# Performance work log

Hardware: AMD Instinct MI355X
Metric: run time of the kernel (lower is better)

The kernel has to match this reference:

```python
import jax, jax.numpy as jnp
import numpy as np

N_ATOMS = 4096
HSIZE = 128
N_HEADS = 8
D_K = HSIZE // N_HEADS


def setup_inputs() -> dict:
    key = jax.random.key(0)
    ks = jax.random.split(key, 11)
    s = 1.0 / np.sqrt(HSIZE)
    return {
        "query": jax.random.normal(ks[0], (N_ATOMS, HSIZE), dtype=jnp.float32),
        "key": jax.random.normal(ks[1], (N_ATOMS, HSIZE), dtype=jnp.float32),
        "value": jax.random.normal(ks[2], (N_ATOMS, HSIZE), dtype=jnp.float32),
        "mask": jax.random.randint(ks[3], (N_ATOMS, N_ATOMS), 0, 2, dtype=jnp.int32),
        "Wq": jax.random.normal(ks[4], (HSIZE, HSIZE), dtype=jnp.float32) * s,
        "bq": jnp.zeros((HSIZE,), dtype=jnp.float32),
        "Wk": jax.random.normal(ks[5], (HSIZE, HSIZE), dtype=jnp.float32) * s,
        "bk": jnp.zeros((HSIZE,), dtype=jnp.float32),
        "Wv": jax.random.normal(ks[6], (HSIZE, HSIZE), dtype=jnp.float32) * s,
        "bv": jnp.zeros((HSIZE,), dtype=jnp.float32),
        "Wo": jax.random.normal(ks[7], (HSIZE, HSIZE), dtype=jnp.float32) * s,
    }


def _mha(query, key, value, mask, Wq, bq, Wk, bk, Wv, bv, Wo):
    n = query.shape[0]
    # project and split heads: [n, hsize] -> [H, n, d_k]
    def heads(x, W, b):
        return (x @ W.T + b).reshape(n, N_HEADS, D_K).transpose(1, 0, 2)
    q = heads(query, Wq, bq)
    k = heads(key, Wk, bk)
    v = heads(value, Wv, bv)
    scale = 1.0 / jnp.sqrt(jnp.asarray(D_K, q.dtype))
    scores = jnp.einsum("hnd,hmd->hnm", q, k) * scale  # [H, n, n]
    scores = jnp.where(mask[None, :, :] == 0, jnp.asarray(-1e9, scores.dtype), scores)
    p_attn = jax.nn.softmax(scores, axis=-1)
    x = jnp.einsum("hnm,hmd->hnd", p_attn, v)  # [H, n, d_k]
    x = x.transpose(1, 0, 2).reshape(n, HSIZE)  # merge heads
    return x @ Wo.T  # output_linear has bias=False


def reference(query, key, value, mask, Wq, bq, Wk, bk, Wv, bv, Wo):
    return _mha(query, key, value, mask, Wq, bq, Wk, bk, Wv, bv, Wo)
```

## Files before the change

### kernel.cpp

```cpp
#include <hip/hip_runtime.h>

#define NA 4096
#define HS 128
#define PSTR 72
#define CSTR 136

typedef unsigned short u16;
typedef unsigned long long u64;
using bf16x8  = __attribute__((ext_vector_type(8))) short;
using f32x4   = __attribute__((ext_vector_type(4))) float;
using ushort8 = __attribute__((ext_vector_type(8))) unsigned short;

#define QSCALE 0.18033688011112042f

static __device__ __forceinline__ u16 f2bf(float f) {
    unsigned u = __builtin_bit_cast(unsigned, f);
    u += 0x7FFFu + ((u >> 16) & 1u);
    return (u16)(u >> 16);
}

__global__ __launch_bounds__(256) void cvt_w(
    const float* __restrict__ Wq, const float* __restrict__ Wk,
    const float* __restrict__ Wv, const float* __restrict__ Wo,
    const float* __restrict__ bq, const float* __restrict__ bk,
    const float* __restrict__ bv, const int* __restrict__ mask,
    u16* __restrict__ Wf, float* __restrict__ bb, u64* __restrict__ Mp)
{
    const int bx = blockIdx.x;
    const int t = threadIdx.x;
    if (bx < 64) {
        const int gid = bx * 256 + t;
        const int e = gid * 4;
        const int mat = e >> 14, off = e & 16383;
        const float* src = (mat == 0) ? Wq : (mat == 1) ? Wk : (mat == 2) ? Wv : Wo;
        const float s = (mat == 0) ? QSCALE : 1.0f;
        float4 v = *(const float4*)(src + off);
        ushort4 o;
        o.x = f2bf(v.x * s); o.y = f2bf(v.y * s);
        o.z = f2bf(v.z * s); o.w = f2bf(v.w * s);
        const int j = off >> 7, k0 = off & 127;
        const int j0 = j >> 4, c = j & 15, kk = k0 >> 5, q = (k0 >> 3) & 3;
        const int tgt = mat * 16384 + ((j0 * 4 + kk) * 16 + c) * 32 + q * 8 + (k0 & 7);
        *(ushort4*)(Wf + tgt) = o;
        if (gid < 128)      bb[gid] = bq[gid] * QSCALE;
        else if (gid < 256) bb[gid] = bk[gid - 128];
        else if (gid < 384) bb[gid] = bv[gid - 256];
    } else {
        const int mb = bx - 64;
        const int wv = t >> 6, lane = t & 63;
        const int row = mb * 4 + wv;
        const int* mrow = mask + (size_t)row * NA;
        u64* orow = Mp + (size_t)row * 64;
#pragma unroll 8
        for (int w = 0; w < 64; ++w) {
            u64 b = __ballot(mrow[w * 64 + lane] != 0);
            if (lane == 0) orow[w] = b;
        }
    }
}

__global__ __launch_bounds__(256) void proj_mfma(
    const float* __restrict__ Xq, const float* __restrict__ Xk, const float* __restrict__ Xv,
    const u16* __restrict__ Wf, const float* __restrict__ bb,
    u16* __restrict__ Qbh, u16* __restrict__ Kbh, u16* __restrict__ VtB)
{
    const int mat = blockIdx.y;
    const float* X = (mat == 0) ? Xq : (mat == 1) ? Xk : Xv;
    const u16* Wm = Wf + mat * 16384;
    const float* bm = bb + mat * 128;
    const int r0b = blockIdx.x * 32;

    __shared__ __align__(16) u16 Xs[32 * CSTR];
    __shared__ __align__(16) u16 Cs[32 * CSTR];

    const int t = threadIdx.x;

    {
        const int r = t >> 3, cb = (t & 7) * 16;
        const float* Xr = X + (size_t)(r0b + r) * HS + cb;
#pragma unroll
        for (int seg = 0; seg < 4; ++seg) {
            float4 f = *(const float4*)(Xr + seg * 4);
            ushort4 u;
            u.x = f2bf(f.x); u.y = f2bf(f.y); u.z = f2bf(f.z); u.w = f2bf(f.w);
            *(ushort4*)(Xs + r * CSTR + cb + seg * 4) = u;
        }
    }
    __syncthreads();

    const int wv = t >> 6, lane = t & 63;
    const int c = lane & 15, q = lane >> 4;
    const int rw = (wv & 1) * 16;
    const int j0b = (wv >> 1) * 4;

    bf16x8 af[4];
#pragma unroll
    for (int kk = 0; kk < 4; ++kk)
        af[kk] = *(const bf16x8*)(Xs + (rw + c) * CSTR + kk * 32 + q * 8);

    const f32x4 zero = {0.f, 0.f, 0.f, 0.f};
#pragma unroll
    for (int jj = 0; jj < 4; ++jj) {
        const int j0 = j0b + jj;
        f32x4 acc = zero;
#pragma unroll
        for (int kk = 0; kk < 4; ++kk) {
            bf16x8 bf = *(const bf16x8*)(Wm + (j0 * 4 + kk) * 512 + c * 32 + q * 8);
            acc = __builtin_amdgcn_mfma_f32_16x16x32_bf16(af[kk], bf, acc, 0, 0, 0);
        }
        const float bias = bm[j0 * 16 + c];
#pragma unroll
        for (int r = 0; r < 4; ++r)
            Cs[(rw + 4 * q + r) * CSTR + j0 * 16 + c] = f2bf(acc[r] + bias);
    }
    __syncthreads();

    if (mat < 2) {
        u16* dst = (mat == 0) ? Qbh : Kbh;
        const int h8 = t >> 5, r = t & 31;
        const u16* src = Cs + r * CSTR + h8 * 16;
        u16* dp = dst + (size_t)h8 * (NA * 16) + (size_t)(r0b + r) * 16;
        *(bf16x8*)(dp)     = *(const bf16x8*)(src);
        *(bf16x8*)(dp + 8) = *(const bf16x8*)(src + 8);
    } else {
        const int d = t >> 1, s = t & 1;
        const int kb = r0b >> 6, ko = (r0b & 32) + s * 16;
        ushort8 v0, v1;
#pragma unroll
        for (int jj = 0; jj < 8; ++jj) v0[jj] = Cs[(s * 16 + jj) * CSTR + d];
#pragma unroll
        for (int jj = 0; jj < 8; ++jj) v1[jj] = Cs[(s * 16 + 8 + jj) * CSTR + d];
        u16* dp = VtB + (size_t)kb * 8192 + d * 64 + ko;
        *(ushort8*)(dp)     = v0;
        *(ushort8*)(dp + 8) = v1;
    }
}

__global__ __launch_bounds__(512, 8) void attn(
    const u64* __restrict__ Mp,
    const u16* __restrict__ Qbh, const u16* __restrict__ Kbh, const u16* __restrict__ VtB,
    float* __restrict__ part)
{
    __shared__ __align__(16) u16 Pbuf[8 * 16 * PSTR];
    __shared__ __align__(8)  u64 Mwp[16 * 17];
    __shared__ __align__(8)  u64 Mtab[16];

    const int t = threadIdx.x;
    const int h = t >> 6;
    const int lane = t & 63;
    const int c = lane & 15;
    const int q = lane >> 4;
    const int tile = blockIdx.x, split = blockIdx.y;
    const int i0 = tile * 16;
    const int kt0 = split * 1024;

    if (t < 256) {
        const int row = t >> 4, w = t & 15;
        Mwp[row * 17 + w] = Mp[(size_t)(i0 + row) * 64 + (kt0 >> 6) + w];
    }
    if (t < 16) {
        const unsigned lo = ((t & 1) ? 0xFFFFu : 0u) | ((t & 2) ? 0xFFFF0000u : 0u);
        const unsigned hi = ((t & 4) ? 0xFFFFu : 0u) | ((t & 8) ? 0xFFFF0000u : 0u);
        Mtab[t] = (u64)lo | ((u64)hi << 32);
    }

    const u16* Qh = Qbh + (size_t)h * (NA * 16);
    const u16* Kh = Kbh + (size_t)h * (NA * 16);

    const bf16x8 qf = *(const bf16x8*)(Qh + (size_t)(i0 + c) * 16 + (q & 1) * 8);

    bf16x8 ones;
#pragma unroll
    for (int i = 0; i < 8; ++i) ones[i] = (short)0x3F80;

    __syncthreads();

    const f32x4 zero = {0.f, 0.f, 0.f, 0.f};
    f32x4 Oacc = zero;
    f32x4 Lacc = zero;
    u16* Pw = Pbuf + h * 16 * PSTR;

    bf16x8 kf[4];
#pragma unroll
    for (int t4 = 0; t4 < 4; ++t4)
        kf[t4] = *(const bf16x8*)(Kh + (size_t)(kt0 + t4 * 16 + c) * 16 + (q & 1) * 8);

#pragma unroll 1
    for (int it = 0; it < 16; ++it) {
        const int kt = kt0 + it * 64;
        const u16* Vb = VtB + (size_t)(kt >> 6) * 8192 + (h * 16 + c) * 64;

        bf16x8 vf0 = *(const bf16x8*)(Vb + q * 8);
        bf16x8 vf1 = *(const bf16x8*)(Vb + 32 + q * 8);

        f32x4 ST[4];
#pragma unroll
        for (int t4 = 0; t4 < 4; ++t4)
            ST[t4] = __builtin_amdgcn_mfma_f32_16x16x32_bf16(kf[t4], qf, zero, 0, 0, 0);

        const int ktn = kt0 + ((it + 1) & 15) * 64;
#pragma unroll
        for (int t4 = 0; t4 < 4; ++t4)
            kf[t4] = *(const bf16x8*)(Kh + (size_t)(ktn + t4 * 16 + c) * 16 + (q & 1) * 8);

        u64 w = Mwp[c * 17 + it] >> (4 * q);
        unsigned mlo = (unsigned)w, mhi = (unsigned)(w >> 32);

#pragma unroll
        for (int t4 = 0; t4 < 4; ++t4) {
            const unsigned mw = (t4 < 2) ? mlo : mhi;
            const int sh = (t4 & 1) * 16;
            const unsigned nib = (mw >> sh) & 15u;
            float p0 = __builtin_amdgcn_exp2f(ST[t4][0]);
            float p1 = __builtin_amdgcn_exp2f(ST[t4][1]);
            float p2 = __builtin_amdgcn_exp2f(ST[t4][2]);
            float p3 = __builtin_amdgcn_exp2f(ST[t4][3]);
            unsigned lo, hi;
            asm("v_cvt_pk_bf16_f32 %0, %1, %2" : "=v"(lo) : "v"(p0), "v"(p1));
            asm("v_cvt_pk_bf16_f32 %0, %1, %2" : "=v"(hi) : "v"(p2), "v"(p3));
            const u64 mex = Mtab[nib];
            lo &= (unsigned)mex;
            hi &= (unsigned)(mex >> 32);
            *(uint2*)(Pw + c * PSTR + t4 * 16 + 4 * q) = make_uint2(lo, hi);
        }
        __asm__ volatile("" ::: "memory");
        __builtin_amdgcn_s_waitcnt(0xC07F);
        __asm__ volatile("" ::: "memory");

        bf16x8 pf0 = *(const bf16x8*)(Pw + c * PSTR + q * 8);
        bf16x8 pf1 = *(const bf16x8*)(Pw + c * PSTR + 32 + q * 8);
        Oacc = __builtin_amdgcn_mfma_f32_16x16x32_bf16(pf0, vf0, Oacc, 0, 0, 0);
        Oacc = __builtin_amdgcn_mfma_f32_16x16x32_bf16(pf1, vf1, Oacc, 0, 0, 0);
        Lacc = __builtin_amdgcn_mfma_f32_16x16x32_bf16(pf0, ones, Lacc, 0, 0, 0);
        Lacc = __builtin_amdgcn_mfma_f32_16x16x32_bf16(pf1, ones, Lacc, 0, 0, 0);
    }

    float* base = part + (size_t)((tile * 4 + split) * 8 + h) * 272;
#pragma unroll
    for (int r = 0; r < 4; ++r)
        base[(4 * q + r) * 16 + c] = Oacc[r];
    if (c == 0) {
#pragma unroll
        for (int r = 0; r < 4; ++r)
            base[256 + 4 * q + r] = Lacc[r];
    }
}

__global__ __launch_bounds__(256) void reduce_out(
    const float* __restrict__ part, const u16* __restrict__ Wf,
    float* __restrict__ out)
{
    __shared__ __align__(16) u16 xs[16 * CSTR];

    const int t = threadIdx.x;
    const int tile = blockIdx.x;
    const int i0 = tile * 16;
    const float* Pt = part + (size_t)tile * 4 * 8 * 272;

    {
        const int i = t >> 4, d = t & 15;
#pragma unroll
        for (int h = 0; h < 8; ++h) {
            float os = 0.f, ls = 0.f;
#pragma unroll
            for (int s = 0; s < 4; ++s) {
                const float* b = Pt + (size_t)(s * 8 + h) * 272;
                os += b[i * 16 + d];
                ls += b[256 + i];
            }
            xs[i * CSTR + h * 16 + d] = f2bf(os / ls);
        }
    }
    __syncthreads();

    const int wv = t >> 6, lane = t & 63;
    const int c = lane & 15, q = lane >> 4;
    const u16* WoB = Wf + 3 * 16384;

    bf16x8 af[4];
#pragma unroll
    for (int kk = 0; kk < 4; ++kk)
        af[kk] = *(const bf16x8*)(xs + c * CSTR + kk * 32 + q * 8);

    const f32x4 zero = {0.f, 0.f, 0.f, 0.f};
#pragma unroll
    for (int jj = 0; jj < 2; ++jj) {
        const int j0 = wv * 2 + jj;
        f32x4 acc = zero;
#pragma unroll
        for (int kk = 0; kk < 4; ++kk) {
            bf16x8 bf = *(const bf16x8*)(WoB + (j0 * 4 + kk) * 512 + c * 32 + q * 8);
            acc = __builtin_amdgcn_mfma_f32_16x16x32_bf16(af[kk], bf, acc, 0, 0, 0);
        }
#pragma unroll
        for (int r = 0; r < 4; ++r)
            out[(size_t)(i0 + 4 * q + r) * HS + j0 * 16 + c] = acc[r];
    }
}

extern "C" void kernel_launch(void* const* d_in, const int* in_sizes, int n_in,
                              void* d_out, int out_size, void* d_ws, size_t ws_size,
                              hipStream_t stream) {
    const float* query = (const float*)d_in[0];
    const float* key   = (const float*)d_in[1];
    const float* value = (const float*)d_in[2];
    const int*   mask  = (const int*)d_in[3];
    const float* Wq    = (const float*)d_in[4];
    const float* bq    = (const float*)d_in[5];
    const float* Wk    = (const float*)d_in[6];
    const float* bk    = (const float*)d_in[7];
    const float* Wv    = (const float*)d_in[8];
    const float* bv    = (const float*)d_in[9];
    const float* Wo    = (const float*)d_in[10];

    u16* Qbh = (u16*)d_ws;
    u16* Kbh = Qbh + (size_t)NA * HS;
    u16* VtB = Kbh + (size_t)NA * HS;
    u16* Wf  = VtB + (size_t)NA * HS;
    float* bb    = (float*)(Wf + 4 * 16384);
    u64*  Mp    = (u64*)(bb + 384);
    float* partb = (float*)(Mp + (size_t)NA * 64);

    cvt_w<<<64 + 1024, 256, 0, stream>>>(Wq, Wk, Wv, Wo, bq, bk, bv, mask, Wf, bb, Mp);
    proj_mfma<<<dim3(128, 3), 256, 0, stream>>>(query, key, value, Wf, bb, Qbh, Kbh, VtB);
    attn<<<dim3(256, 4), 512, 0, stream>>>(Mp, Qbh, Kbh, VtB, partb);
    reduce_out<<<256, 256, 0, stream>>>(partb, Wf, (float*)d_out);
}
```

Baseline: 203.0 us.

## Keep P in registers via permuted K layout; fuse mask packing into projection

K rows are written in a permuted order so the S^T MFMA output lanes line up with the A-operand layout of the PV MFMA. P is then assembled in registers, which removes the LDS write, the waitcnt and the readback. Mask bit-packing moves from the weight-convert kernel into the projection launch, so mask packing overlaps with the projection GEMM. It also adds s_setprio around the MFMA groups and relaxes the occupancy hint in launch_bounds; the risk is a mismatch between the permuted K layout and the mask bit indexing.

Result: faster. 194.7 us (-4.1%).

```diff
diff --git a/kernel.cpp b/kernel.cpp
--- a/kernel.cpp
+++ b/kernel.cpp
@@ -2,7 +2,6 @@
 
 #define NA 4096
 #define HS 128
-#define PSTR 72
 #define CSTR 136
 
 typedef unsigned short u16;
@@ -10,6 +9,7 @@
 using bf16x8  = __attribute__((ext_vector_type(8))) short;
 using f32x4   = __attribute__((ext_vector_type(4))) float;
 using ushort8 = __attribute__((ext_vector_type(8))) unsigned short;
+using u32x4   = __attribute__((ext_vector_type(4))) unsigned;
 
 #define QSCALE 0.18033688011112042f
 
@@ -23,30 +23,39 @@
     const float* __restrict__ Wq, const float* __restrict__ Wk,
     const float* __restrict__ Wv, const float* __restrict__ Wo,
     const float* __restrict__ bq, const float* __restrict__ bk,
-    const float* __restrict__ bv, const int* __restrict__ mask,
-    u16* __restrict__ Wf, float* __restrict__ bb, u64* __restrict__ Mp)
+    const float* __restrict__ bv,
+    u16* __restrict__ Wf, float* __restrict__ bb)
 {
-    const int bx = blockIdx.x;
+    const int gid = blockIdx.x * 256 + threadIdx.x;
+    const int e = gid * 4;
+    const int mat = e >> 14, off = e & 16383;
+    const float* src = (mat == 0) ? Wq : (mat == 1) ? Wk : (mat == 2) ? Wv : Wo;
+    const float s = (mat == 0) ? QSCALE : 1.0f;
+    float4 v = *(const float4*)(src + off);
+    ushort4 o;
+    o.x = f2bf(v.x * s); o.y = f2bf(v.y * s);
+    o.z = f2bf(v.z * s); o.w = f2bf(v.w * s);
+    const int j = off >> 7, k0 = off & 127;
+    const int j0 = j >> 4, c = j & 15, kk = k0 >> 5, q = (k0 >> 3) & 3;
+    const int tgt = mat * 16384 + ((j0 * 4 + kk) * 16 + c) * 32 + q * 8 + (k0 & 7);
+    *(ushort4*)(Wf + tgt) = o;
+    if (gid < 128)      bb[gid] = bq[gid] * QSCALE;
+    else if (gid < 256) bb[gid] = bk[gid - 128];
+    else if (gid < 384) bb[gid] = bv[gid - 256];
+}
+
+__global__ __launch_bounds__(256) void proj_mfma(
+    const float* __restrict__ Xq, const float* __restrict__ Xk, const float* __restrict__ Xv,
+    const u16* __restrict__ Wf, const float* __restrict__ bb,
+    const int* __restrict__ mask,
+    u16* __restrict__ Qbh, u16* __restrict__ Kbh, u16* __restrict__ VtB,
+    u64* __restrict__ Mp)
+{
+    const int blk = blockIdx.x;
     const int t = threadIdx.x;
-    if (bx < 64) {
-        const int gid = bx * 256 + t;
-        const int e = gid * 4;
-        const int mat = e >> 14, off = e & 16383;
-        const float* src = (mat == 0) ? Wq : (mat == 1) ? Wk : (mat == 2) ? Wv : Wo;
-        const float s = (mat == 0) ? QSCALE : 1.0f;
-        float4 v = *(const float4*)(src + off);
-        ushort4 o;
-        o.x = f2bf(v.x * s); o.y = f2bf(v.y * s);
-        o.z = f2bf(v.z * s); o.w = f2bf(v.w * s);
-        const int j = off >> 7, k0 = off & 127;
-        const int j0 = j >> 4, c = j & 15, kk = k0 >> 5, q = (k0 >> 3) & 3;
-        const int tgt = mat * 16384 + ((j0 * 4 + kk) * 16 + c) * 32 + q * 8 + (k0 & 7);
-        *(ushort4*)(Wf + tgt) = o;
-        if (gid < 128)      bb[gid] = bq[gid] * QSCALE;
-        else if (gid < 256) bb[gid] = bk[gid - 128];
-        else if (gid < 384) bb[gid] = bv[gid - 256];
-    } else {
-        const int mb = bx - 64;
+
+    if (blk >= 384) {
+        const int mb = blk - 384;
         const int wv = t >> 6, lane = t & 63;
         const int row = mb * 4 + wv;
         const int* mrow = mask + (size_t)row * NA;
@@ -56,24 +65,17 @@
             u64 b = __ballot(mrow[w * 64 + lane] != 0);
             if (lane == 0) orow[w] = b;
         }
-    }
-}
-
-__global__ __launch_bounds__(256) void proj_mfma(
-    const float* __restrict__ Xq, const float* __restrict__ Xk, const float* __restrict__ Xv,
-    const u16* __restrict__ Wf, const float* __restrict__ bb,
-    u16* __restrict__ Qbh, u16* __restrict__ Kbh, u16* __restrict__ VtB)
-{
-    const int mat = blockIdx.y;
+        return;
+    }
+
+    const int mat = blk >> 7;
     const float* X = (mat == 0) ? Xq : (mat == 1) ? Xk : Xv;
     const u16* Wm = Wf + mat * 16384;
     const float* bm = bb + mat * 128;
-    const int r0b = blockIdx.x * 32;
+    const int r0b = (blk & 127) * 32;
 
     __shared__ __align__(16) u16 Xs[32 * CSTR];
     __shared__ __align__(16) u16 Cs[32 * CSTR];
-
-    const int t = threadIdx.x;
 
     {
         const int r = t >> 3, cb = (t & 7) * 16;
@@ -119,7 +121,14 @@
         u16* dst = (mat == 0) ? Qbh : Kbh;
         const int h8 = t >> 5, r = t & 31;
         const u16* src = Cs + r * CSTR + h8 * 16;
-        u16* dp = dst + (size_t)h8 * (NA * 16) + (size_t)(r0b + r) * 16;
+        int drow = r0b + r;
+        if (mat == 1) {
+            const int k = (r0b & 32) + r;
+            const int slot = ((k >> 5) * 2 + ((k >> 2) & 1)) * 16
+                           + ((k >> 3) & 3) * 4 + (k & 3);
+            drow = (r0b & ~63) + slot;
+        }
+        u16* dp = dst + (size_t)h8 * (NA * 16) + (size_t)drow * 16;
         *(bf16x8*)(dp)     = *(const bf16x8*)(src);
         *(bf16x8*)(dp + 8) = *(const bf16x8*)(src + 8);
     } else {
@@ -136,12 +145,11 @@
     }
 }
 
-__global__ __launch_bounds__(512, 8) void attn(
+__global__ __launch_bounds__(512, 4) void attn(
     const u64* __restrict__ Mp,
     const u16* __restrict__ Qbh, const u16* __restrict__ Kbh, const u16* __restrict__ VtB,
     float* __restrict__ part)
 {
-    __shared__ __align__(16) u16 Pbuf[8 * 16 * PSTR];
     __shared__ __align__(8)  u64 Mwp[16 * 17];
     __shared__ __align__(8)  u64 Mtab[16];
 
@@ -178,7 +186,6 @@
     const f32x4 zero = {0.f, 0.f, 0.f, 0.f};
     f32x4 Oacc = zero;
     f32x4 Lacc = zero;
-    u16* Pw = Pbuf + h * 16 * PSTR;
 
     bf16x8 kf[4];
 #pragma unroll
@@ -194,23 +201,25 @@
         bf16x8 vf1 = *(const bf16x8*)(Vb + 32 + q * 8);
 
         f32x4 ST[4];
+        __builtin_amdgcn_s_setprio(1);
 #pragma unroll
         for (int t4 = 0; t4 < 4; ++t4)
             ST[t4] = __builtin_amdgcn_mfma_f32_16x16x32_bf16(kf[t4], qf, zero, 0, 0, 0);
+        __builtin_amdgcn_s_setprio(0);
 
         const int ktn = kt0 + ((it + 1) & 15) * 64;
 #pragma unroll
         for (int t4 = 0; t4 < 4; ++t4)
             kf[t4] = *(const bf16x8*)(Kh + (size_t)(ktn + t4 * 16 + c) * 16 + (q & 1) * 8);
 
-        u64 w = Mwp[c * 17 + it] >> (4 * q);
-        unsigned mlo = (unsigned)w, mhi = (unsigned)(w >> 32);
-
+        const u64 w = Mwp[c * 17 + it];
+        const unsigned wa = (unsigned)(w >> (8 * q));
+        const unsigned wb = (unsigned)(w >> (32 + 8 * q));
+
+        unsigned pl[4], ph[4];
 #pragma unroll
         for (int t4 = 0; t4 < 4; ++t4) {
-            const unsigned mw = (t4 < 2) ? mlo : mhi;
-            const int sh = (t4 & 1) * 16;
-            const unsigned nib = (mw >> sh) & 15u;
+            const unsigned nib = (((t4 & 2) ? wb : wa) >> ((t4 & 1) * 4)) & 15u;
             float p0 = __builtin_amdgcn_exp2f(ST[t4][0]);
             float p1 = __builtin_amdgcn_exp2f(ST[t4][1]);
             float p2 = __builtin_amdgcn_exp2f(ST[t4][2]);
@@ -219,20 +228,20 @@
             asm("v_cvt_pk_bf16_f32 %0, %1, %2" : "=v"(lo) : "v"(p0), "v"(p1));
             asm("v_cvt_pk_bf16_f32 %0, %1, %2" : "=v"(hi) : "v"(p2), "v"(p3));
             const u64 mex = Mtab[nib];
-            lo &= (unsigned)mex;
-            hi &= (unsigned)(mex >> 32);
-            *(uint2*)(Pw + c * PSTR + t4 * 16 + 4 * q) = make_uint2(lo, hi);
-        }
-        __asm__ volatile("" ::: "memory");
-        __builtin_amdgcn_s_waitcnt(0xC07F);
-        __asm__ volatile("" ::: "memory");
-
-        bf16x8 pf0 = *(const bf16x8*)(Pw + c * PSTR + q * 8);
-        bf16x8 pf1 = *(const bf16x8*)(Pw + c * PSTR + 32 + q * 8);
+            pl[t4] = lo & (unsigned)mex;
+            ph[t4] = hi & (unsigned)(mex >> 32);
+        }
+        const u32x4 a0 = { pl[0], ph[0], pl[1], ph[1] };
+        const u32x4 a1 = { pl[2], ph[2], pl[3], ph[3] };
+        const bf16x8 pf0 = __builtin_bit_cast(bf16x8, a0);
+        const bf16x8 pf1 = __builtin_bit_cast(bf16x8, a1);
+
+        __builtin_amdgcn_s_setprio(1);
         Oacc = __builtin_amdgcn_mfma_f32_16x16x32_bf16(pf0, vf0, Oacc, 0, 0, 0);
         Oacc = __builtin_amdgcn_mfma_f32_16x16x32_bf16(pf1, vf1, Oacc, 0, 0, 0);
         Lacc = __builtin_amdgcn_mfma_f32_16x16x32_bf16(pf0, ones, Lacc, 0, 0, 0);
         Lacc = __builtin_amdgcn_mfma_f32_16x16x32_bf16(pf1, ones, Lacc, 0, 0, 0);
+        __builtin_amdgcn_s_setprio(0);
     }
 
     float* base = part + (size_t)((tile * 4 + split) * 8 + h) * 272;
@@ -321,8 +330,9 @@
     u64*  Mp    = (u64*)(bb + 384);
     float* partb = (float*)(Mp + (size_t)NA * 64);
 
-    cvt_w<<<64 + 1024, 256, 0, stream>>>(Wq, Wk, Wv, Wo, bq, bk, bv, mask, Wf, bb, Mp);
-    proj_mfma<<<dim3(128, 3), 256, 0, stream>>>(query, key, value, Wf, bb, Qbh, Kbh, VtB);
+    cvt_w<<<64, 256, 0, stream>>>(Wq, Wk, Wv, Wo, bq, bk, bv, Wf, bb);
+    proj_mfma<<<384 + 1024, 256, 0, stream>>>(query, key, value, Wf, bb, mask,
+                                              Qbh, Kbh, VtB, Mp);
     attn<<<dim3(256, 4), 512, 0, stream>>>(Mp, Qbh, Kbh, VtB, partb);
     reduce_out<<<256, 256, 0, stream>>>(partb, Wf, (float*)d_out);
 }
```
